# Kernel tuning notes

Measured on AMD Instinct MI355X. Metric: run time of the kernel, lower is better.

The kernel has to match this reference:

```python
import jax, jax.numpy as jnp
import numpy as np

BATCH, DIN, DSTATE, SEQLEN = 4, 2048, 16, 2048


def setup_inputs() -> dict:
    key = jax.random.key(0)
    ks = jax.random.split(key, 7)
    u = jax.random.normal(ks[0], (BATCH, DIN, SEQLEN), dtype=jnp.float32)
    # delta pre-softplus; moderate positive-ish values like Mamba dt_proj output
    delta = jax.random.uniform(ks[1], (BATCH, DIN, SEQLEN), dtype=jnp.float32, minval=-2.0, maxval=1.0)
    # A is negative in real Mamba (A = -exp(A_log)); keep recurrence stable
    A = -jnp.exp(jax.random.uniform(ks[2], (DIN, DSTATE), dtype=jnp.float32, minval=-1.0, maxval=1.0))
    B = jax.random.normal(ks[3], (BATCH, DSTATE, SEQLEN), dtype=jnp.float32)
    C = jax.random.normal(ks[4], (BATCH, DSTATE, SEQLEN), dtype=jnp.float32)
    D = jax.random.normal(ks[5], (DIN,), dtype=jnp.float32)
    z = jax.random.normal(ks[6], (BATCH, DIN, SEQLEN), dtype=jnp.float32)
    return {"u": u, "delta": delta, "A": A, "B": B, "C": C, "D": D, "z": z}


def reference(u, delta, A, B, C, D, z):
    """Mamba selective scan (selective_scan_ref semantics, delta_softplus=True).

    u, delta, z: (b, d, l); A: (d, n); B, C: (b, n, l); D: (d,).
    y_t = C_t . x_t + D*u_t, x_t = exp(dt_t*A)*x_{t-1} + dt_t*B_t*u_t,
    final y gated by SiLU(z).
    """
    dt = jax.nn.softplus(delta)                      # (b, d, l)

    def step(x, inp):
        dt_t, u_t, B_t, C_t = inp                    # (b,d) (b,d) (b,n) (b,n)
        dA = jnp.exp(dt_t[..., None] * A)            # (b, d, n)
        x = x * dA + (dt_t * u_t)[..., None] * B_t[:, None, :]
        y_t = jnp.einsum('bdn,bn->bd', x, C_t)
        return x, y_t

    xs = (jnp.moveaxis(dt, -1, 0),                   # (l, b, d)
          jnp.moveaxis(u, -1, 0),
          jnp.moveaxis(B, -1, 0),                    # (l, b, n)
          jnp.moveaxis(C, -1, 0))
    x0 = jnp.zeros((u.shape[0], u.shape[1], A.shape[1]), dtype=u.dtype)
    _, ys = jax.lax.scan(step, x0, xs)               # ys: (l, b, d)
    y = jnp.moveaxis(ys, 0, -1)                      # (b, d, l)
    y = y + D[None, :, None] * u
    y = y * (z * jax.nn.sigmoid(z))                  # SiLU gate
    return y
```

## Files before the change

### kernel.cpp

```cpp
#include <hip/hip_runtime.h>


#define BATCHSZ 4
#define DIN 2048
#define NSTATE 16
#define SEQ 2048
#define NCH (BATCHSZ * DIN)
#define NGRP (NCH / 256)
#define SUB 16
#define ST 20
#define L2E 1.44269504f

__device__ __forceinline__ float softplus_f(float v) {
    float e = __builtin_amdgcn_exp2f(v * L2E);
    return 0.69314718f * __builtin_amdgcn_logf(1.0f + e);
}

__device__ __forceinline__ float silu_f(float v) {
    float s = __builtin_amdgcn_rcpf(1.0f + __builtin_amdgcn_exp2f(-v * L2E));
    return v * s;
}

__device__ __forceinline__ float comp4(const float4& f, int k) {
    return k == 0 ? f.x : k == 1 ? f.y : k == 2 ? f.z : f.w;
}

__device__ __forceinline__ void set4(float4& f, int k, float v) {
    if (k == 0) f.x = v; else if (k == 1) f.y = v; else if (k == 2) f.z = v; else f.w = v;
}


template<int NC>
__global__ __launch_bounds__(256, 3) void k_pass1(
        const float* __restrict__ u, const float* __restrict__ delta,
        const float* __restrict__ A, const float* __restrict__ Bm,
        float* __restrict__ wsq, float* __restrict__ wsS) {
    constexpr int LC = SEQ / NC;
    constexpr int NSUB = LC / SUB;
    __shared__ float Ub[256 * ST];
    __shared__ float Db[256 * ST];
    __shared__ float Bc[LC * 20];

    int tid = threadIdx.x;
    int w6 = tid & ~63;
    int l = tid & 63;
    int g = blockIdx.x & (NGRP - 1);
    int c = blockIdx.x >> 5;
    int chBase = g << 8;
    int b = chBase >> 11;
    int bd = chBase + tid;
    int d = bd & (DIN - 1);

    const float* ug = u + (size_t)chBase * SEQ + (size_t)c * LC;
    const float* dg = delta + (size_t)chBase * SEQ + (size_t)c * LC;
    const float* Bg = Bm + (size_t)b * NSTATE * SEQ + (size_t)c * LC;

    #pragma unroll
    for (int i = 0; i < LC * NSTATE / 256; ++i) {
        int e = i * 256 + tid;
        int n = e / LC;
        int t = e - n * LC;
        Bc[t * 20 + n] = Bg[(size_t)n * SEQ + t];
    }

    float A2[NSTATE];
    {
        const float* Ar = A + (size_t)d * NSTATE;
        #pragma unroll
        for (int n = 0; n < NSTATE; ++n) A2[n] = Ar[n] * L2E;
    }
    float x[NSTATE];
    #pragma unroll
    for (int n = 0; n < NSTATE; ++n) x[n] = 0.0f;
    float S = 0.0f;

    __syncthreads();

    for (int st = 0; st < NSUB; ++st) {
        int tb = st * SUB;
        #pragma unroll
        for (int it = 0; it < 4; ++it) {
            int r = w6 + it * 16 + (l >> 2);
            int cq = (l & 3) << 2;
            *(float4*)(&Ub[r * ST + cq]) = *(const float4*)(ug + (size_t)r * SEQ + tb + cq);
            *(float4*)(&Db[r * ST + cq]) = *(const float4*)(dg + (size_t)r * SEQ + tb + cq);
        }
        #pragma unroll
        for (int t4 = 0; t4 < SUB / 4; ++t4) {
            float4 u4 = *(const float4*)(&Ub[tid * ST + t4 * 4]);
            float4 d4 = *(const float4*)(&Db[tid * ST + t4 * 4]);
            #pragma unroll
            for (int k = 0; k < 4; ++k) {
                float dt = softplus_f(comp4(d4, k));
                S += dt;
                float du = dt * comp4(u4, k);
                int t = tb + t4 * 4 + k;
                const float4* Br = (const float4*)(&Bc[t * 20]);
                float bb[NSTATE];
                *(float4*)&bb[0] = Br[0]; *(float4*)&bb[4] = Br[1];
                *(float4*)&bb[8] = Br[2]; *(float4*)&bb[12] = Br[3];
                #pragma unroll
                for (int n = 0; n < NSTATE; ++n) {
                    float dA = __builtin_amdgcn_exp2f(A2[n] * dt);
                    x[n] = x[n] * dA + du * bb[n];
                }
            }
        }
    }

    #pragma unroll
    for (int n = 0; n < NSTATE; ++n) wsq[((size_t)n * NC + c) * NCH + bd] = x[n];
    wsS[(size_t)c * NCH + bd] = S;
}

template<int NC>
__global__ __launch_bounds__(256) void k_pass2(
        const float* __restrict__ A, float* __restrict__ wsq,
        float* __restrict__ wsS) {
    int idx = blockIdx.x * 256 + threadIdx.x;
    int n = idx >> 13;
    int bd = idx & (NCH - 1);
    int d = bd & (DIN - 1);

    float A2 = A[(size_t)d * NSTATE + n] * L2E;
    float x = 0.0f;
    float* qbase = wsq + (size_t)n * NC * NCH + bd;

    for (int c0 = 0; c0 < NC; c0 += 4) {
        float S0 = wsS[(size_t)(c0 + 0) * NCH + bd];
        float S1 = wsS[(size_t)(c0 + 1) * NCH + bd];
        float S2 = wsS[(size_t)(c0 + 2) * NCH + bd];
        float S3 = wsS[(size_t)(c0 + 3) * NCH + bd];
        float* p0 = qbase + (size_t)(c0 + 0) * NCH;
        float* p1 = qbase + (size_t)(c0 + 1) * NCH;
        float* p2 = qbase + (size_t)(c0 + 2) * NCH;
        float* p3 = qbase + (size_t)(c0 + 3) * NCH;
        float q0 = *p0, q1 = *p1, q2 = *p2, q3 = *p3;
        float t0 = x; x = x * __builtin_amdgcn_exp2f(A2 * S0) + q0;
        float t1 = x; x = x * __builtin_amdgcn_exp2f(A2 * S1) + q1;
        float t2 = x; x = x * __builtin_amdgcn_exp2f(A2 * S2) + q2;
        float t3 = x; x = x * __builtin_amdgcn_exp2f(A2 * S3) + q3;
        *p0 = t0; *p1 = t1; *p2 = t2; *p3 = t3;
    }
}

template<int NC>
__global__ __launch_bounds__(256, 3) void k_pass3(
        const float* __restrict__ u, const float* __restrict__ delta,
        const float* __restrict__ A, const float* __restrict__ Bm,
        const float* __restrict__ Cm, const float* __restrict__ Dv,
        const float* __restrict__ z, const float* __restrict__ wsq,
        float* __restrict__ out) {
    constexpr int LC = SEQ / NC;
    constexpr int NSUB = LC / SUB;
    __shared__ float Ub[256 * ST];
    __shared__ float Db[256 * ST];
    __shared__ float Bc[LC * 20];
    __shared__ float Cc[LC * 20];

    int tid = threadIdx.x;
    int w6 = tid & ~63;
    int l = tid & 63;
    int g = blockIdx.x & (NGRP - 1);
    int c = blockIdx.x >> 5;
    int chBase = g << 8;
    int b = chBase >> 11;
    int bd = chBase + tid;
    int d = bd & (DIN - 1);

    const float* ug = u + (size_t)chBase * SEQ + (size_t)c * LC;
    const float* dg = delta + (size_t)chBase * SEQ + (size_t)c * LC;
    const float* zg = z + (size_t)chBase * SEQ + (size_t)c * LC;
    float* og = out + (size_t)chBase * SEQ + (size_t)c * LC;
    const float* Bg = Bm + (size_t)b * NSTATE * SEQ + (size_t)c * LC;
    const float* Cg = Cm + (size_t)b * NSTATE * SEQ + (size_t)c * LC;

    #pragma unroll
    for (int i = 0; i < LC * NSTATE / 256; ++i) {
        int e = i * 256 + tid;
        int n = e / LC;
        int t = e - n * LC;
        Bc[t * 20 + n] = Bg[(size_t)n * SEQ + t];
        Cc[t * 20 + n] = Cg[(size_t)n * SEQ + t];
    }

    float A2[NSTATE];
    {
        const float* Ar = A + (size_t)d * NSTATE;
        #pragma unroll
        for (int n = 0; n < NSTATE; ++n) A2[n] = Ar[n] * L2E;
    }
    float x[NSTATE];
    #pragma unroll
    for (int n = 0; n < NSTATE; ++n)
        x[n] = wsq[((size_t)n * NC + c) * NCH + bd];
    float Dd = Dv[d];

    __syncthreads();

    for (int st = 0; st < NSUB; ++st) {
        int tb = st * SUB;
        float4 zr[4];
        #pragma unroll
        for (int it = 0; it < 4; ++it) {
            int r = w6 + it * 16 + (l >> 2);
            int cq = (l & 3) << 2;
            *(float4*)(&Ub[r * ST + cq]) = *(const float4*)(ug + (size_t)r * SEQ + tb + cq);
            *(float4*)(&Db[r * ST + cq]) = *(const float4*)(dg + (size_t)r * SEQ + tb + cq);
            zr[it] = *(const float4*)(zg + (size_t)r * SEQ + tb + cq);
        }
        #pragma unroll
        for (int t4 = 0; t4 < SUB / 4; ++t4) {
            float4 u4 = *(const float4*)(&Ub[tid * ST + t4 * 4]);
            float4 d4 = *(const float4*)(&Db[tid * ST + t4 * 4]);
            float4 y4;
            #pragma unroll
            for (int k = 0; k < 4; ++k) {
                float uv = comp4(u4, k);
                float dt = softplus_f(comp4(d4, k));
                float du = dt * uv;
                int t = tb + t4 * 4 + k;
                const float4* Br = (const float4*)(&Bc[t * 20]);
                const float4* Cr = (const float4*)(&Cc[t * 20]);
                float bb[NSTATE], cc[NSTATE];
                *(float4*)&bb[0] = Br[0]; *(float4*)&bb[4] = Br[1];
                *(float4*)&bb[8] = Br[2]; *(float4*)&bb[12] = Br[3];
                *(float4*)&cc[0] = Cr[0]; *(float4*)&cc[4] = Cr[1];
                *(float4*)&cc[8] = Cr[2]; *(float4*)&cc[12] = Cr[3];
                float acc = 0.0f;
                #pragma unroll
                for (int n = 0; n < NSTATE; ++n) {
                    float dA = __builtin_amdgcn_exp2f(A2[n] * dt);
                    x[n] = x[n] * dA + du * bb[n];
                    acc += x[n] * cc[n];
                }
                set4(y4, k, acc + Dd * uv);
            }
            *(float4*)(&Ub[tid * ST + t4 * 4]) = y4;
        }
        #pragma unroll
        for (int it = 0; it < 4; ++it) {
            int r = w6 + it * 16 + (l >> 2);
            int cq = (l & 3) << 2;
            float4 y4 = *(const float4*)(&Ub[r * ST + cq]);
            float4 oo;
            #pragma unroll
            for (int k = 0; k < 4; ++k)
                set4(oo, k, comp4(y4, k) * silu_f(comp4(zr[it], k)));
            *(float4*)(og + (size_t)r * SEQ + tb + cq) = oo;
        }
    }
}

__global__ __launch_bounds__(256) void k_simple(
        const float* __restrict__ u, const float* __restrict__ delta,
        const float* __restrict__ A, const float* __restrict__ Bm,
        const float* __restrict__ Cm, const float* __restrict__ Dv,
        const float* __restrict__ z, float* __restrict__ out) {
    int bd = blockIdx.x * 256 + threadIdx.x;
    int b  = bd >> 11;
    int d  = bd & (DIN - 1);

    float A2[NSTATE];
    const float* Ar = A + d * NSTATE;
    #pragma unroll
    for (int n = 0; n < NSTATE; ++n) A2[n] = Ar[n] * L2E;
    float x[NSTATE];
    #pragma unroll
    for (int n = 0; n < NSTATE; ++n) x[n] = 0.0f;

    float Dd = Dv[d];
    size_t base = (size_t)bd * SEQ;
    const float4* u4 = (const float4*)(u + base);
    const float4* d4 = (const float4*)(delta + base);
    const float4* z4 = (const float4*)(z + base);
    float4* o4 = (float4*)(out + base);
    const float* Bp = Bm + (size_t)b * NSTATE * SEQ;
    const float* Cp = Cm + (size_t)b * NSTATE * SEQ;

    for (int t4 = 0; t4 < SEQ / 4; ++t4) {
        float4 uu = u4[t4];
        float4 dd = d4[t4];
        float4 zz = z4[t4];
        float4 yy;
        #pragma unroll
        for (int k = 0; k < 4; ++k) {
            float uvk = comp4(uu, k);
            float dt = softplus_f(comp4(dd, k));
            float du = dt * uvk;
            int t = t4 * 4 + k;
            float acc = 0.0f;
            #pragma unroll
            for (int n = 0; n < NSTATE; ++n) {
                float dA = __builtin_amdgcn_exp2f(A2[n] * dt);
                x[n] = x[n] * dA + du * Bp[n * SEQ + t];
                acc += x[n] * Cp[n * SEQ + t];
            }
            float y = acc + Dd * uvk;
            y = y * silu_f(comp4(zz, k));
            set4(yy, k, y);
        }
        o4[t4] = yy;
    }
}

template<int NC>
static void launch_chunked(const float* u, const float* delta, const float* A,
                           const float* Bm, const float* Cm, const float* Dv,
                           const float* z, float* ws, float* out, hipStream_t stream) {
    float* wsq = ws;
    float* wsS = ws + (size_t)NSTATE * NC * NCH;
    k_pass1<NC><<<NGRP * NC, 256, 0, stream>>>(u, delta, A, Bm, wsq, wsS);
    k_pass2<NC><<<(NSTATE * NCH) / 256, 256, 0, stream>>>(A, wsq, wsS);
    k_pass3<NC><<<NGRP * NC, 256, 0, stream>>>(u, delta, A, Bm, Cm, Dv, z, wsq, out);
}

extern "C" void kernel_launch(void* const* d_in, const int* in_sizes, int n_in,
                              void* d_out, int out_size, void* d_ws, size_t ws_size,
                              hipStream_t stream) {
    const float* u     = (const float*)d_in[0];
    const float* delta = (const float*)d_in[1];
    const float* A     = (const float*)d_in[2];
    const float* Bm    = (const float*)d_in[3];
    const float* Cm    = (const float*)d_in[4];
    const float* Dv    = (const float*)d_in[5];
    const float* z     = (const float*)d_in[6];
    float* out = (float*)d_out;
    float* ws = (float*)d_ws;

    size_t need64 = (size_t)(NSTATE + 1) * 64 * NCH * sizeof(float);
    size_t need32 = (size_t)(NSTATE + 1) * 32 * NCH * sizeof(float);
    size_t need16 = (size_t)(NSTATE + 1) * 16 * NCH * sizeof(float);
    if (ws_size >= need64) {
        launch_chunked<64>(u, delta, A, Bm, Cm, Dv, z, ws, out, stream);
    } else if (ws_size >= need32) {
        launch_chunked<32>(u, delta, A, Bm, Cm, Dv, z, ws, out, stream);
    } else if (ws_size >= need16) {
        launch_chunked<16>(u, delta, A, Bm, Cm, Dv, z, ws, out, stream);
    } else {
        k_simple<<<NCH / 256, 256, 0, stream>>>(u, delta, A, Bm, Cm, Dv, z, out);
    }
}
```

Baseline: 369.1 us.

## Pre-transpose B/C globally, stream u/delta via async LDS DMA with swizzle

Adds a small kernel that transposes B and C into time-major layout in the workspace, so the scan kernels read B/C rows directly from global/cache instead of staging them in shared memory. u and delta are now copied into LDS with global_load_lds DMA using an XOR-swizzled 32-step tile, and the next tile is issued after the current compute. Chunk count is fixed at 16, occupancy hint raised to 4, and the pass2 loop is unrolled. The risks are extra launch and workspace traffic, serialized waits on vmcnt(0), and B/C loads going through global memory rather than LDS.

```diff
diff --git a/kernel.cpp b/kernel.cpp
--- a/kernel.cpp
+++ b/kernel.cpp
@@ -7,8 +7,10 @@
 #define SEQ 2048
 #define NCH (BATCHSZ * DIN)
 #define NGRP (NCH / 256)
-#define SUB 16
-#define ST 20
+#define NC 16
+#define LC (SEQ / NC)
+#define SUB 32
+#define NSUB (LC / SUB)
 #define L2E 1.44269504f
 
 __device__ __forceinline__ float softplus_f(float v) {
@@ -29,39 +31,57 @@
     if (k == 0) f.x = v; else if (k == 1) f.y = v; else if (k == 2) f.z = v; else f.w = v;
 }
 
-
-template<int NC>
-__global__ __launch_bounds__(256, 3) void k_pass1(
+__device__ __forceinline__ void dma16(const float* g, float* l) {
+    __builtin_amdgcn_global_load_lds(
+        (const __attribute__((address_space(1))) void*)g,
+        (__attribute__((address_space(3))) void*)l, 16, 0, 0);
+}
+
+
+__global__ __launch_bounds__(256) void k_transBC(
+        const float* __restrict__ Bm, const float* __restrict__ Cm,
+        float* __restrict__ Bt, float* __restrict__ Ct) {
+    int idx = blockIdx.x * 256 + threadIdx.x;
+    int b = idx >> 11;
+    int t = idx & (SEQ - 1);
+    const float* sb = Bm + (size_t)b * NSTATE * SEQ + t;
+    const float* sc = Cm + (size_t)b * NSTATE * SEQ + t;
+    float* db = Bt + ((size_t)b * SEQ + t) * NSTATE;
+    float* dc = Ct + ((size_t)b * SEQ + t) * NSTATE;
+    #pragma unroll
+    for (int m = 0; m < 4; ++m) {
+        float4 v, w;
+        v.x = sb[(size_t)(m * 4 + 0) * SEQ]; w.x = sc[(size_t)(m * 4 + 0) * SEQ];
+        v.y = sb[(size_t)(m * 4 + 1) * SEQ]; w.y = sc[(size_t)(m * 4 + 1) * SEQ];
+        v.z = sb[(size_t)(m * 4 + 2) * SEQ]; w.z = sc[(size_t)(m * 4 + 2) * SEQ];
+        v.w = sb[(size_t)(m * 4 + 3) * SEQ]; w.w = sc[(size_t)(m * 4 + 3) * SEQ];
+        *(float4*)(db + m * 4) = v;
+        *(float4*)(dc + m * 4) = w;
+    }
+}
+
+__global__ __launch_bounds__(256, 4) void k_pass1(
         const float* __restrict__ u, const float* __restrict__ delta,
-        const float* __restrict__ A, const float* __restrict__ Bm,
+        const float* __restrict__ A, const float* __restrict__ Bt,
         float* __restrict__ wsq, float* __restrict__ wsS) {
-    constexpr int LC = SEQ / NC;
-    constexpr int NSUB = LC / SUB;
-    __shared__ float Ub[256 * ST];
-    __shared__ float Db[256 * ST];
-    __shared__ float Bc[LC * 20];
+    __shared__ float Ub[256 * 32];
+    __shared__ float Db[256 * 32];
 
     int tid = threadIdx.x;
+    int l = tid & 63;
     int w6 = tid & ~63;
-    int l = tid & 63;
     int g = blockIdx.x & (NGRP - 1);
     int c = blockIdx.x >> 5;
     int chBase = g << 8;
     int b = chBase >> 11;
     int bd = chBase + tid;
     int d = bd & (DIN - 1);
+    int rowA = w6 + (l >> 3);
+    int lq = l & 7;
 
     const float* ug = u + (size_t)chBase * SEQ + (size_t)c * LC;
     const float* dg = delta + (size_t)chBase * SEQ + (size_t)c * LC;
-    const float* Bg = Bm + (size_t)b * NSTATE * SEQ + (size_t)c * LC;
-
-    #pragma unroll
-    for (int i = 0; i < LC * NSTATE / 256; ++i) {
-        int e = i * 256 + tid;
-        int n = e / LC;
-        int t = e - n * LC;
-        Bc[t * 20 + n] = Bg[(size_t)n * SEQ + t];
-    }
+    const float* Btc = Bt + ((size_t)b * SEQ + (size_t)c * LC) * NSTATE;
 
     float A2[NSTATE];
     {
@@ -74,31 +94,31 @@
     for (int n = 0; n < NSTATE; ++n) x[n] = 0.0f;
     float S = 0.0f;
 
-    __syncthreads();
+    #pragma unroll
+    for (int it = 0; it < 8; ++it) {
+        int r = rowA + it * 8;
+        int q = lq ^ (r & 7);
+        dma16(ug + (size_t)r * SEQ + q * 4, &Ub[(w6 + it * 8) * 32]);
+        dma16(dg + (size_t)r * SEQ + q * 4, &Db[(w6 + it * 8) * 32]);
+    }
 
     for (int st = 0; st < NSUB; ++st) {
-        int tb = st * SUB;
-        #pragma unroll
-        for (int it = 0; it < 4; ++it) {
-            int r = w6 + it * 16 + (l >> 2);
-            int cq = (l & 3) << 2;
-            *(float4*)(&Ub[r * ST + cq]) = *(const float4*)(ug + (size_t)r * SEQ + tb + cq);
-            *(float4*)(&Db[r * ST + cq]) = *(const float4*)(dg + (size_t)r * SEQ + tb + cq);
-        }
-        #pragma unroll
-        for (int t4 = 0; t4 < SUB / 4; ++t4) {
-            float4 u4 = *(const float4*)(&Ub[tid * ST + t4 * 4]);
-            float4 d4 = *(const float4*)(&Db[tid * ST + t4 * 4]);
+        asm volatile("s_waitcnt vmcnt(0)" ::: "memory");
+        __builtin_amdgcn_sched_barrier(0);
+        #pragma unroll
+        for (int t4 = 0; t4 < 8; ++t4) {
+            int ph = (t4 ^ (tid & 7)) * 4;
+            float4 u4 = *(const float4*)(&Ub[tid * 32 + ph]);
+            float4 d4 = *(const float4*)(&Db[tid * 32 + ph]);
+            const float4* Br = (const float4*)(Btc + (size_t)(st * SUB + t4 * 4) * NSTATE);
             #pragma unroll
             for (int k = 0; k < 4; ++k) {
                 float dt = softplus_f(comp4(d4, k));
                 S += dt;
                 float du = dt * comp4(u4, k);
-                int t = tb + t4 * 4 + k;
-                const float4* Br = (const float4*)(&Bc[t * 20]);
                 float bb[NSTATE];
-                *(float4*)&bb[0] = Br[0]; *(float4*)&bb[4] = Br[1];
-                *(float4*)&bb[8] = Br[2]; *(float4*)&bb[12] = Br[3];
+                *(float4*)&bb[0] = Br[k * 4 + 0]; *(float4*)&bb[4] = Br[k * 4 + 1];
+                *(float4*)&bb[8] = Br[k * 4 + 2]; *(float4*)&bb[12] = Br[k * 4 + 3];
                 #pragma unroll
                 for (int n = 0; n < NSTATE; ++n) {
                     float dA = __builtin_amdgcn_exp2f(A2[n] * dt);
@@ -106,6 +126,17 @@
                 }
             }
         }
+        if (st + 1 < NSUB) {
+            __builtin_amdgcn_sched_barrier(0);
+            int tb = (st + 1) * SUB;
+            #pragma unroll
+            for (int it = 0; it < 8; ++it) {
+                int r = rowA + it * 8;
+                int q = lq ^ (r & 7);
+                dma16(ug + (size_t)r * SEQ + tb + q * 4, &Ub[(w6 + it * 8) * 32]);
+                dma16(dg + (size_t)r * SEQ + tb + q * 4, &Db[(w6 + it * 8) * 32]);
+            }
+        }
     }
 
     #pragma unroll
@@ -113,7 +144,6 @@
     wsS[(size_t)c * NCH + bd] = S;
 }
 
-template<int NC>
 __global__ __launch_bounds__(256) void k_pass2(
         const float* __restrict__ A, float* __restrict__ wsq,
         float* __restrict__ wsS) {
@@ -126,6 +156,7 @@
     float x = 0.0f;
     float* qbase = wsq + (size_t)n * NC * NCH + bd;
 
+    #pragma unroll
     for (int c0 = 0; c0 < NC; c0 += 4) {
         float S0 = wsS[(size_t)(c0 + 0) * NCH + bd];
         float S1 = wsS[(size_t)(c0 + 1) * NCH + bd];
@@ -144,45 +175,33 @@
     }
 }
 
-template<int NC>
-__global__ __launch_bounds__(256, 3) void k_pass3(
+__global__ __launch_bounds__(256, 4) void k_pass3(
         const float* __restrict__ u, const float* __restrict__ delta,
-        const float* __restrict__ A, const float* __restrict__ Bm,
-        const float* __restrict__ Cm, const float* __restrict__ Dv,
+        const float* __restrict__ A, const float* __restrict__ Bt,
+        const float* __restrict__ Ct, const float* __restrict__ Dv,
         const float* __restrict__ z, const float* __restrict__ wsq,
         float* __restrict__ out) {
-    constexpr int LC = SEQ / NC;
-    constexpr int NSUB = LC / SUB;
-    __shared__ float Ub[256 * ST];
-    __shared__ float Db[256 * ST];
-    __shared__ float Bc[LC * 20];
-    __shared__ float Cc[LC * 20];
+    __shared__ float Ub[256 * 32];
+    __shared__ float Db[256 * 32];
 
     int tid = threadIdx.x;
+    int l = tid & 63;
     int w6 = tid & ~63;
-    int l = tid & 63;
     int g = blockIdx.x & (NGRP - 1);
     int c = blockIdx.x >> 5;
     int chBase = g << 8;
     int b = chBase >> 11;
     int bd = chBase + tid;
     int d = bd & (DIN - 1);
+    int rowA = w6 + (l >> 3);
+    int lq = l & 7;
 
     const float* ug = u + (size_t)chBase * SEQ + (size_t)c * LC;
     const float* dg = delta + (size_t)chBase * SEQ + (size_t)c * LC;
     const float* zg = z + (size_t)chBase * SEQ + (size_t)c * LC;
     float* og = out + (size_t)chBase * SEQ + (size_t)c * LC;
-    const float* Bg = Bm + (size_t)b * NSTATE * SEQ + (size_t)c * LC;
-    const float* Cg = Cm + (size_t)b * NSTATE * SEQ + (size_t)c * LC;
-
-    #pragma unroll
-    for (int i = 0; i < LC * NSTATE / 256; ++i) {
-        int e = i * 256 + tid;
-        int n = e / LC;
-        int t = e - n * LC;
-        Bc[t * 20 + n] = Bg[(size_t)n * SEQ + t];
-        Cc[t * 20 + n] = Cg[(size_t)n * SEQ + t];
-    }
+    const float* Btc = Bt + ((size_t)b * SEQ + (size_t)c * LC) * NSTATE;
+    const float* Ctc = Ct + ((size_t)b * SEQ + (size_t)c * LC) * NSTATE;
 
     float A2[NSTATE];
     {
@@ -196,37 +215,36 @@
         x[n] = wsq[((size_t)n * NC + c) * NCH + bd];
     float Dd = Dv[d];
 
-    __syncthreads();
+    #pragma unroll
+    for (int it = 0; it < 8; ++it) {
+        int r = rowA + it * 8;
+        int q = lq ^ (r & 7);
+        dma16(ug + (size_t)r * SEQ + q * 4, &Ub[(w6 + it * 8) * 32]);
+        dma16(dg + (size_t)r * SEQ + q * 4, &Db[(w6 + it * 8) * 32]);
+    }
 
     for (int st = 0; st < NSUB; ++st) {
         int tb = st * SUB;
-        float4 zr[4];
-        #pragma unroll
-        for (int it = 0; it < 4; ++it) {
-            int r = w6 + it * 16 + (l >> 2);
-            int cq = (l & 3) << 2;
-            *(float4*)(&Ub[r * ST + cq]) = *(const float4*)(ug + (size_t)r * SEQ + tb + cq);
-            *(float4*)(&Db[r * ST + cq]) = *(const float4*)(dg + (size_t)r * SEQ + tb + cq);
-            zr[it] = *(const float4*)(zg + (size_t)r * SEQ + tb + cq);
-        }
-        #pragma unroll
-        for (int t4 = 0; t4 < SUB / 4; ++t4) {
-            float4 u4 = *(const float4*)(&Ub[tid * ST + t4 * 4]);
-            float4 d4 = *(const float4*)(&Db[tid * ST + t4 * 4]);
+        asm volatile("s_waitcnt vmcnt(0)" ::: "memory");
+        __builtin_amdgcn_sched_barrier(0);
+        #pragma unroll
+        for (int t4 = 0; t4 < 8; ++t4) {
+            int ph = (t4 ^ (tid & 7)) * 4;
+            float4 u4 = *(const float4*)(&Ub[tid * 32 + ph]);
+            float4 d4 = *(const float4*)(&Db[tid * 32 + ph]);
+            const float4* Br = (const float4*)(Btc + (size_t)(tb + t4 * 4) * NSTATE);
+            const float4* Cr = (const float4*)(Ctc + (size_t)(tb + t4 * 4) * NSTATE);
             float4 y4;
             #pragma unroll
             for (int k = 0; k < 4; ++k) {
                 float uv = comp4(u4, k);
                 float dt = softplus_f(comp4(d4, k));
                 float du = dt * uv;
-                int t = tb + t4 * 4 + k;
-                const float4* Br = (const float4*)(&Bc[t * 20]);
-                const float4* Cr = (const float4*)(&Cc[t * 20]);
                 float bb[NSTATE], cc[NSTATE];
-                *(float4*)&bb[0] = Br[0]; *(float4*)&bb[4] = Br[1];
-                *(float4*)&bb[8] = Br[2]; *(float4*)&bb[12] = Br[3];
-                *(float4*)&cc[0] = Cr[0]; *(float4*)&cc[4] = Cr[1];
-                *(float4*)&cc[8] = Cr[2]; *(float4*)&cc[12] = Cr[3];
+                *(float4*)&bb[0] = Br[k * 4 + 0]; *(float4*)&bb[4] = Br[k * 4 + 1];
+                *(float4*)&bb[8] = Br[k * 4 + 2]; *(float4*)&bb[12] = Br[k * 4 + 3];
+                *(float4*)&cc[0] = Cr[k * 4 + 0]; *(float4*)&cc[4] = Cr[k * 4 + 1];
+                *(float4*)&cc[8] = Cr[k * 4 + 2]; *(float4*)&cc[12] = Cr[k * 4 + 3];
                 float acc = 0.0f;
                 #pragma unroll
                 for (int n = 0; n < NSTATE; ++n) {
@@ -236,18 +254,30 @@
                 }
                 set4(y4, k, acc + Dd * uv);
             }
-            *(float4*)(&Ub[tid * ST + t4 * 4]) = y4;
-        }
-        #pragma unroll
-        for (int it = 0; it < 4; ++it) {
-            int r = w6 + it * 16 + (l >> 2);
-            int cq = (l & 3) << 2;
-            float4 y4 = *(const float4*)(&Ub[r * ST + cq]);
+            *(float4*)(&Ub[tid * 32 + ph]) = y4;
+        }
+        #pragma unroll
+        for (int it = 0; it < 8; ++it) {
+            int r = rowA + it * 8;
+            int sq = (lq ^ (r & 7)) * 4;
+            float4 y4 = *(const float4*)(&Ub[r * 32 + sq]);
+            float4 z4 = *(const float4*)(zg + (size_t)r * SEQ + tb + lq * 4);
             float4 oo;
             #pragma unroll
             for (int k = 0; k < 4; ++k)
-                set4(oo, k, comp4(y4, k) * silu_f(comp4(zr[it], k)));
-            *(float4*)(og + (size_t)r * SEQ + tb + cq) = oo;
+                set4(oo, k, comp4(y4, k) * silu_f(comp4(z4, k)));
+            *(float4*)(og + (size_t)r * SEQ + tb + lq * 4) = oo;
+        }
+        if (st + 1 < NSUB) {
+            __builtin_amdgcn_sched_barrier(0);
+            int tb2 = tb + SUB;
+            #pragma unroll
+            for (int it = 0; it < 8; ++it) {
+                int r = rowA + it * 8;
+                int q = lq ^ (r & 7);
+                dma16(ug + (size_t)r * SEQ + tb2 + q * 4, &Ub[(w6 + it * 8) * 32]);
+                dma16(dg + (size_t)r * SEQ + tb2 + q * 4, &Db[(w6 + it * 8) * 32]);
+            }
         }
     }
 }
@@ -302,17 +332,6 @@
         }
         o4[t4] = yy;
     }
-}
-
-template<int NC>
-static void launch_chunked(const float* u, const float* delta, const float* A,
-                           const float* Bm, const float* Cm, const float* Dv,
-                           const float* z, float* ws, float* out, hipStream_t stream) {
-    float* wsq = ws;
-    float* wsS = ws + (size_t)NSTATE * NC * NCH;
-    k_pass1<NC><<<NGRP * NC, 256, 0, stream>>>(u, delta, A, Bm, wsq, wsS);
-    k_pass2<NC><<<(NSTATE * NCH) / 256, 256, 0, stream>>>(A, wsq, wsS);
-    k_pass3<NC><<<NGRP * NC, 256, 0, stream>>>(u, delta, A, Bm, Cm, Dv, z, wsq, out);
 }
 
 extern "C" void kernel_launch(void* const* d_in, const int* in_sizes, int n_in,
@@ -328,15 +347,20 @@
     float* out = (float*)d_out;
     float* ws = (float*)d_ws;
 
-    size_t need64 = (size_t)(NSTATE + 1) * 64 * NCH * sizeof(float);
-    size_t need32 = (size_t)(NSTATE + 1) * 32 * NCH * sizeof(float);
-    size_t need16 = (size_t)(NSTATE + 1) * 16 * NCH * sizeof(float);
-    if (ws_size >= need64) {
-        launch_chunked<64>(u, delta, A, Bm, Cm, Dv, z, ws, out, stream);
-    } else if (ws_size >= need32) {
-        launch_chunked<32>(u, delta, A, Bm, Cm, Dv, z, ws, out, stream);
-    } else if (ws_size >= need16) {
-        launch_chunked<16>(u, delta, A, Bm, Cm, Dv, z, ws, out, stream);
+    size_t nq = (size_t)NSTATE * NC * NCH;
+    size_t ns = (size_t)NC * NCH;
+    size_t nt = (size_t)BATCHSZ * SEQ * NSTATE;
+    size_t need = (nq + ns + 2 * nt) * sizeof(float);
+
+    if (ws_size >= need) {
+        float* wsq = ws;
+        float* wsS = wsq + nq;
+        float* Bt  = wsS + ns;
+        float* Ct  = Bt + nt;
+        k_transBC<<<(BATCHSZ * SEQ) / 256, 256, 0, stream>>>(Bm, Cm, Bt, Ct);
+        k_pass1<<<NGRP * NC, 256, 0, stream>>>(u, delta, A, Bt, wsq, wsS);
+        k_pass2<<<(NSTATE * NCH) / 256, 256, 0, stream>>>(A, wsq, wsS);
+        k_pass3<<<NGRP * NC, 256, 0, stream>>>(u, delta, A, Bt, Ct, Dv, z, wsq, out);
     } else {
         k_simple<<<NCH / 256, 256, 0, stream>>>(u, delta, A, Bm, Cm, Dv, z, out);
     }
```

Measured after the change: 386.9 us. 1.05x slower.
